# Kernel tuning notes

Measured on AMD Instinct MI355X. Metric: run time of the kernel, lower is better.

## Reference

```python
import jax, jax.numpy as jnp
import numpy as np
from math import pi

# Layer dims for num_inputs=0, width=64, depth=5, num_outputs=3
CHANNELS = [4, 64, 64, 64, 64, 3]

def _splits():
    biases, weights, idx = [], [], 0
    for l in range(len(CHANNELS) - 1):
        nci, nco = CHANNELS[l], CHANNELS[l + 1]
        biases.append((idx, idx + nco)); idx += nco
        weights.append((idx, idx + nci * nco)); idx += nci * nco
    return biases, weights, idx

BIASES, WEIGHTS, NUM_PARAMS = _splits()  # NUM_PARAMS == 12995


def _get_coords(h, w, ds):
    """Faithful port of _get_coords, including the original's bug where the
    y-channels reuse the normalized x coordinate vector (requires h == w)."""
    scale = 7.0 / 8.0
    x = jnp.arange(w, dtype=jnp.float32)
    y = jnp.arange(h, dtype=jnp.float32)
    x_c = (jnp.remainder(x, ds) / ds)
    y_c = (jnp.remainder(y, ds) / ds)
    x_c = x_c / (x_c.max() / scale)          # x_cos == x_sin in original
    y_cn = x_c / (y_c.max() / scale)          # bug: built from x_c
    xcos = jnp.cos(2.0 * pi * x_c)
    xsin = jnp.sin(2.0 * pi * x_c)
    ycos = jnp.cos(2.0 * pi * y_cn)           # length w, laid out along h (h==w)
    ysin = jnp.sin(2.0 * pi * y_cn)
    row = lambda v: jnp.broadcast_to(v[None, :], (h, w))
    col = lambda v: jnp.broadcast_to(v[:, None], (h, w))
    return jnp.stack([row(xcos), row(xsin), col(ycos), col(ysin)], axis=0)  # (4,h,w)


def setup_inputs() -> dict:
    key = jax.random.key(0)
    k1, k2 = jax.random.split(key)
    highres = jax.random.normal(k1, (2, 4, 512, 512), dtype=jnp.float32)
    lr_params = jax.random.normal(k2, (2, NUM_PARAMS, 64, 64), dtype=jnp.float32)
    return {"highres": highres, "lr_params": lr_params}


def reference(highres, lr_params):
    bs, _, h, w = highres.shape
    h_lr, w_lr = lr_params.shape[2], lr_params.shape[3]
    k = h // h_lr  # tile size

    coords = _get_coords(h, w, k)                       # (4, h, w)
    pe = jnp.broadcast_to(coords[None], (bs, 4, h, w))  # highres is overwritten by PE

    # unfold into (bs, h_lr, w_lr, k*k, 4) tiles
    tiles = pe.reshape(bs, 4, h_lr, k, w_lr, k)
    tiles = tiles.transpose(0, 2, 4, 3, 5, 1).reshape(bs, h_lr, w_lr, k * k, 4)

    out = tiles
    num_layers = len(CHANNELS) - 1
    for idx in range(num_layers):
        nci, nco = CHANNELS[idx], CHANNELS[idx + 1]
        b0, b1 = BIASES[idx]
        w0, w1 = WEIGHTS[idx]
        w_ = lr_params[:, w0:w1].transpose(0, 2, 3, 1).reshape(bs, h_lr, w_lr, nci, nco)
        b_ = lr_params[:, b0:b1].transpose(0, 2, 3, 1)[:, :, :, None, :]  # (bs,h_lr,w_lr,1,nco)
        out = jnp.einsum('bhwpi,bhwio->bhwpo', out, w_) + b_
        if idx < num_layers - 1:
            out = jnp.where(out >= 0, out, 0.01 * out)  # leaky_relu(0.01)
        else:
            out = jnp.tanh(out)

    out = out.reshape(bs, h_lr, w_lr, k, k, CHANNELS[-1])
    out = out.transpose(0, 5, 1, 3, 2, 4).reshape(bs, CHANNELS[-1], h, w)
    return out
```

## Files before the change

kernel.cpp:

```cpp
#include <hip/hip_runtime.h>
#include <math.h>


static constexpr int PLANE = 4096;
static constexpr int NPAR  = 12995;
static constexpr int WROW  = 160;
static constexpr int AHI   = 8192;

__device__ __forceinline__ float leaky(float v) { return fmaxf(v, 0.01f * v); }

__device__ __forceinline__ constexpr float cx(int k) {
  constexpr float R = 0.70710678118654752f;
  const float t[8] = {1.f, R, 0.f, -R, -1.f, -R, 0.f, R};
  return t[k];
}
__device__ __forceinline__ constexpr float sx(int k) {
  constexpr float R = 0.70710678118654752f;
  const float t[8] = {0.f, R, 1.f, R, 0.f, -R, -1.f, -R};
  return t[k];
}

__global__ __launch_bounds__(256, 1) void pqn(const float* __restrict__ lr,
                                              float* __restrict__ out) {
  __shared__ alignas(16) float A[2 * AHI];
  __shared__ alignas(16) float WB[4][4 * WROW];

  const int tid = threadIdx.x;
  const int j   = tid & 3;
  const int pg  = (tid >> 2) & 7;
  const int cob = tid >> 5;

  const int n  = blockIdx.x;
  const int e2 = (n >> 3) & 3;
  const int P  = (n & 7) | ((n >> 5) << 3);
  const int jg = ((P & 3) << 2) | e2;
  const int i  = (P >> 2) & 63;
  const int b  = (P >> 8) & 1;

  const float* __restrict__ wb =
      lr + (size_t)b * NPAR * PLANE + (size_t)(i * 64 + jg * 4);
  const float* __restrict__ pt = wb + j;

  float fyc, fys;
  sincosf(0.78539816339744830962f * pg, &fys, &fyc);

  const int abase = pg * 16 + j * 4;
  const int wrow  = j * WROW;
  const int sq    = tid >> 7;
  const int sc    = tid & 127;

  float4 sA, sB;
  {
    const size_t cb = 384;
    sA = *(const float4*)(wb + (cb + tid) * PLANE);
    sB = *(const float4*)(wb + (cb + 256 + tid) * PLANE);
  }
  float l0b[8], l0w[32], bb[8];
#pragma unroll
  for (int m = 0; m < 8; ++m) l0b[m] = pt[(size_t)(cob * 8 + m) * PLANE];
#pragma unroll
  for (int f = 0; f < 4; ++f)
#pragma unroll
    for (int m = 0; m < 8; ++m)
      l0w[f * 8 + m] = pt[(size_t)(64 + f * 64 + cob * 8 + m) * PLANE];
#pragma unroll
  for (int m = 0; m < 8; ++m) bb[m] = pt[(size_t)(320 + cob * 8 + m) * PLANE];

#pragma unroll
  for (int col = 0; col < 8; ++col) {
    float t[8];
#pragma unroll
    for (int k = 0; k < 8; ++k) {
      float v = l0b[col];
      v = fmaf(cx(k), l0w[col], v);
      v = fmaf(sx(k), l0w[8 + col], v);
      v = fmaf(fyc,  l0w[16 + col], v);
      v = fmaf(fys,  l0w[24 + col], v);
      t[k] = leaky(v);
    }
    float4 v0, v1;
    v0.x = t[0]; v0.y = t[1]; v0.z = t[2]; v0.w = t[3];
    v1.x = t[4]; v1.y = t[5]; v1.z = t[6]; v1.w = t[7];
    *(float4*)&A[(cob * 8 + col) * 128 + abase]       = v0;
    *(float4*)&A[(cob * 8 + col) * 128 + abase + AHI] = v1;
  }
#pragma unroll
  for (int jj = 0; jj < 4; ++jj) {
    WB[sq][jj * WROW + sc]     = ((const float*)&sA)[jj];
    WB[2 + sq][jj * WROW + sc] = ((const float*)&sB)[jj];
  }
  asm volatile("s_waitcnt lgkmcnt(0)" ::: "memory");
  __builtin_amdgcn_s_barrier();
  __builtin_amdgcn_sched_barrier(0);

  float y[64];
#pragma unroll
  for (int m = 0; m < 64; ++m) y[m] = 0.f;

#pragma unroll 1
  for (int g = 0; g < 24; ++g) {
    if (g < 23) {
      const int gn = g + 1;
      const size_t cb = 384 + (size_t)(gn >> 3) * 4160 + (size_t)(gn & 7) * 512;
      sA = *(const float4*)(wb + (cb + tid) * PLANE);
      sB = *(const float4*)(wb + (cb + 256 + tid) * PLANE);
    }
    const int r0 = (g & 7) * 8;
#pragma unroll
    for (int q = 0; q < 4; ++q) {
      const float* Wt = WB[q];
#pragma unroll
      for (int cl = 0; cl < 2; ++cl) {
        const int ci = r0 + q * 2 + cl;
        const float4 a0 = *(const float4*)&A[ci * 128 + abase];
        const float4 a1 = *(const float4*)&A[ci * 128 + abase + AHI];
        const float4 w0 = *(const float4*)&Wt[wrow + cl * 64 + cob * 8];
        const float4 w1 = *(const float4*)&Wt[wrow + cl * 64 + cob * 8 + 4];
        const float av[8] = {a0.x, a0.y, a0.z, a0.w, a1.x, a1.y, a1.z, a1.w};
        const float wv[8] = {w0.x, w0.y, w0.z, w0.w, w1.x, w1.y, w1.z, w1.w};
#pragma unroll
        for (int col = 0; col < 8; ++col)
#pragma unroll
          for (int k = 0; k < 8; ++k)
            y[col * 8 + k] = fmaf(av[k], wv[col], y[col * 8 + k]);
      }
    }
    asm volatile("s_waitcnt lgkmcnt(0)" ::: "memory");
    __builtin_amdgcn_s_barrier();
    __builtin_amdgcn_sched_barrier(0);

    if ((g & 7) == 7) {
      const int l = g >> 3;
#pragma unroll
      for (int col = 0; col < 8; ++col) {
        float4 v0, v1;
        v0.x = leaky(y[col * 8 + 0] + bb[col]);
        v0.y = leaky(y[col * 8 + 1] + bb[col]);
        v0.z = leaky(y[col * 8 + 2] + bb[col]);
        v0.w = leaky(y[col * 8 + 3] + bb[col]);
        v1.x = leaky(y[col * 8 + 4] + bb[col]);
        v1.y = leaky(y[col * 8 + 5] + bb[col]);
        v1.z = leaky(y[col * 8 + 6] + bb[col]);
        v1.w = leaky(y[col * 8 + 7] + bb[col]);
        *(float4*)&A[(cob * 8 + col) * 128 + abase]       = v0;
        *(float4*)&A[(cob * 8 + col) * 128 + abase + AHI] = v1;
      }
#pragma unroll
      for (int m = 0; m < 64; ++m) y[m] = 0.f;
      if (l < 2) {
#pragma unroll
        for (int m = 0; m < 8; ++m)
          bb[m] = pt[(size_t)(320 + (l + 1) * 4160 + cob * 8 + m) * PLANE];
      }
    }
    if (g < 23) {
#pragma unroll
      for (int jj = 0; jj < 4; ++jj) {
        WB[sq][jj * WROW + sc]     = ((const float*)&sA)[jj];
        WB[2 + sq][jj * WROW + sc] = ((const float*)&sB)[jj];
      }
    }
    asm volatile("s_waitcnt lgkmcnt(0)" ::: "memory");
    __builtin_amdgcn_s_barrier();
    __builtin_amdgcn_sched_barrier(0);
  }

  float po[24];
#pragma unroll
  for (int m = 0; m < 24; ++m) po[m] = 0.f;
#pragma unroll
  for (int cl = 0; cl < 8; ++cl) {
    const int ci = cob * 8 + cl;
    const float4 a0 = *(const float4*)&A[ci * 128 + abase];
    const float4 a1 = *(const float4*)&A[ci * 128 + abase + AHI];
#pragma unroll
    for (int o = 0; o < 3; ++o) {
      const float w = pt[(size_t)(12803 + ci * 3 + o) * PLANE];
      po[o * 8 + 0] = fmaf(a0.x, w, po[o * 8 + 0]);
      po[o * 8 + 1] = fmaf(a0.y, w, po[o * 8 + 1]);
      po[o * 8 + 2] = fmaf(a0.z, w, po[o * 8 + 2]);
      po[o * 8 + 3] = fmaf(a0.w, w, po[o * 8 + 3]);
      po[o * 8 + 4] = fmaf(a1.x, w, po[o * 8 + 4]);
      po[o * 8 + 5] = fmaf(a1.y, w, po[o * 8 + 5]);
      po[o * 8 + 6] = fmaf(a1.z, w, po[o * 8 + 6]);
      po[o * 8 + 7] = fmaf(a1.w, w, po[o * 8 + 7]);
    }
  }
  asm volatile("s_waitcnt lgkmcnt(0)" ::: "memory");
  __builtin_amdgcn_s_barrier();
  float* R = A;
#pragma unroll
  for (int m = 0; m < 24; m += 4)
    *(float4*)&R[tid * 28 + m] = *(float4*)&po[m];
  asm volatile("s_waitcnt lgkmcnt(0)" ::: "memory");
  __builtin_amdgcn_s_barrier();
  __builtin_amdgcn_sched_barrier(0);

  if (cob == 0) {
#pragma unroll
    for (int o = 0; o < 3; ++o) {
      const float bias = pt[(size_t)(12800 + o) * PLANE];
      float s[8];
#pragma unroll
      for (int k = 0; k < 8; ++k) s[k] = bias;
#pragma unroll
      for (int cb = 0; cb < 8; ++cb) {
#pragma unroll
        for (int k = 0; k < 8; ++k)
          s[k] += R[(cb * 32 + tid) * 28 + o * 8 + k];
      }
      float4 v0, v1;
      v0.x = tanhf(s[0]); v0.y = tanhf(s[1]); v0.z = tanhf(s[2]); v0.w = tanhf(s[3]);
      v1.x = tanhf(s[4]); v1.y = tanhf(s[5]); v1.z = tanhf(s[6]); v1.w = tanhf(s[7]);
      float* op = out + (size_t)b * 786432 + (size_t)o * 262144 +
                  (size_t)(i * 8 + pg) * 512 + (size_t)((jg * 4 + j) * 8);
      *(float4*)op = v0;
      *(float4*)(op + 4) = v1;
    }
  }
}

extern "C" void kernel_launch(void* const* d_in, const int* in_sizes, int n_in,
                              void* d_out, int out_size, void* d_ws, size_t ws_size,
                              hipStream_t stream) {
  (void)in_sizes; (void)n_in; (void)d_ws; (void)ws_size; (void)out_size;
  const float* lr = (const float*)d_in[1];
  float* out = (float*)d_out;
  hipLaunchKernelGGL(pqn, dim3(2048), dim3(256), 0, stream, lr, out);
}
```

Before: 252.2 us.

## Deepen weight prefetch to two stages ahead and pad WB row stride

Measured after the change: 364.5 us. 44.5% more time.

```diff
diff --git a/kernel.cpp b/kernel.cpp
--- a/kernel.cpp
+++ b/kernel.cpp
@@ -4,7 +4,7 @@
 
 static constexpr int PLANE = 4096;
 static constexpr int NPAR  = 12995;
-static constexpr int WROW  = 160;
+static constexpr int WROW  = 164;
 static constexpr int AHI   = 8192;
 
 __device__ __forceinline__ float leaky(float v) { return fmaxf(v, 0.01f * v); }
@@ -49,11 +49,15 @@
   const int sq    = tid >> 7;
   const int sc    = tid & 127;
 
-  float4 sA, sB;
+  auto gaddr = [&](int g) -> size_t {
+    return 384 + (size_t)(g >> 3) * 4160 + (size_t)(g & 7) * 512;
+  };
+
+  float4 pA0, pB0, pA1, pB1;
   {
-    const size_t cb = 384;
-    sA = *(const float4*)(wb + (cb + tid) * PLANE);
-    sB = *(const float4*)(wb + (cb + 256 + tid) * PLANE);
+    const size_t cb = gaddr(0);
+    pA0 = *(const float4*)(wb + (cb + tid) * PLANE);
+    pB0 = *(const float4*)(wb + (cb + 256 + tid) * PLANE);
   }
   float l0b[8], l0w[32], bb[8];
 #pragma unroll
@@ -86,8 +90,16 @@
   }
 #pragma unroll
   for (int jj = 0; jj < 4; ++jj) {
-    WB[sq][jj * WROW + sc]     = ((const float*)&sA)[jj];
-    WB[2 + sq][jj * WROW + sc] = ((const float*)&sB)[jj];
+    WB[sq][jj * WROW + sc]     = ((const float*)&pA0)[jj];
+    WB[2 + sq][jj * WROW + sc] = ((const float*)&pB0)[jj];
+  }
+  {
+    size_t cb = gaddr(1);
+    pA0 = *(const float4*)(wb + (cb + tid) * PLANE);
+    pB0 = *(const float4*)(wb + (cb + 256 + tid) * PLANE);
+    cb = gaddr(2);
+    pA1 = *(const float4*)(wb + (cb + tid) * PLANE);
+    pB1 = *(const float4*)(wb + (cb + 256 + tid) * PLANE);
   }
   asm volatile("s_waitcnt lgkmcnt(0)" ::: "memory");
   __builtin_amdgcn_s_barrier();
@@ -99,12 +111,6 @@
 
 #pragma unroll 1
   for (int g = 0; g < 24; ++g) {
-    if (g < 23) {
-      const int gn = g + 1;
-      const size_t cb = 384 + (size_t)(gn >> 3) * 4160 + (size_t)(gn & 7) * 512;
-      sA = *(const float4*)(wb + (cb + tid) * PLANE);
-      sB = *(const float4*)(wb + (cb + 256 + tid) * PLANE);
-    }
     const int r0 = (g & 7) * 8;
 #pragma unroll
     for (int q = 0; q < 4; ++q) {
@@ -153,12 +159,21 @@
           bb[m] = pt[(size_t)(320 + (l + 1) * 4160 + cob * 8 + m) * PLANE];
       }
     }
-    if (g < 23) {
+    if (g + 1 < 24) {
+      const float4& wA = (g & 1) ? pA1 : pA0;
+      const float4& wB = (g & 1) ? pB1 : pB0;
 #pragma unroll
       for (int jj = 0; jj < 4; ++jj) {
-        WB[sq][jj * WROW + sc]     = ((const float*)&sA)[jj];
-        WB[2 + sq][jj * WROW + sc] = ((const float*)&sB)[jj];
-      }
+        WB[sq][jj * WROW + sc]     = ((const float*)&wA)[jj];
+        WB[2 + sq][jj * WROW + sc] = ((const float*)&wB)[jj];
+      }
+    }
+    if (g + 3 < 24) {
+      const size_t cb = gaddr(g + 3);
+      float4& wA = (g & 1) ? pA1 : pA0;
+      float4& wB = (g & 1) ? pB1 : pB0;
+      wA = *(const float4*)(wb + (cb + tid) * PLANE);
+      wB = *(const float4*)(wb + (cb + 256 + tid) * PLANE);
     }
     asm volatile("s_waitcnt lgkmcnt(0)" ::: "memory");
     __builtin_amdgcn_s_barrier();
```
